# Optimization experiments

Hardware: AMD Instinct MI355X
Metric: run time of the kernel (lower is better)

## Reference

```python
import jax, jax.numpy as jnp
import numpy as np

TOP_K = 2  # matches init k


def setup_inputs() -> dict:
    key = jax.random.key(0)
    ks = jax.random.split(key, 5)
    B, S, D, E, H = 2, 2048, 1024, 8, 4096
    scale = 0.02
    return {
        "x": jax.random.normal(ks[0], (B, S, D), dtype=jnp.float32),
        "wg": jax.random.normal(ks[1], (D, E), dtype=jnp.float32) * scale,
        "w1": jax.random.normal(ks[2], (E, D, H), dtype=jnp.float32) * scale,
        "w3": jax.random.normal(ks[3], (E, D, H), dtype=jnp.float32) * scale,
        "w2": jax.random.normal(ks[4], (E, H, D), dtype=jnp.float32) * scale,
    }


def reference(x, wg, w1, w3, w2):
    # x: [B, S, D]; wg: [D, E]; w1/w3: [E, D, H]; w2: [E, H, D]
    B, S, D = x.shape
    E = wg.shape[1]
    T = B * S
    xt = x.reshape(T, D)

    # Top-k gating: softmax over expert logits, keep top-k, renormalize.
    logits = xt @ wg                                    # [T, E]
    probs = jax.nn.softmax(logits, axis=-1)             # [T, E]
    topv, topi = jax.lax.top_k(probs, TOP_K)            # [T, k]
    topv = topv / topv.sum(axis=-1, keepdims=True)
    # Dense combine weights [T, E] (zero for non-selected experts).
    comb = jnp.zeros((T, E), dtype=x.dtype).at[jnp.arange(T)[:, None], topi].set(topv)

    # Per-expert SwiGLU MLP with weighted combine (loop over small fixed E).
    out = jnp.zeros_like(xt)
    for e in range(E):
        h = jax.nn.silu(xt @ w1[e]) * (xt @ w3[e])      # [T, H]
        out = out + comb[:, e:e + 1] * (h @ w2[e])       # [T, D]
    return out.reshape(B, S, D)
```

## Files before the change

kernel.cpp:

```cpp
#include <hip/hip_runtime.h>
#include <cstdint>
#include <cstddef>

#define T_TOK 4096
#define DIM   1024
#define NEXP  8
#define HDIM  4096
#define NSLOT (2 * T_TOK)

#define BM 128
#define BN 128
#define BK 32

typedef __attribute__((ext_vector_type(8))) short s16x8;
typedef __attribute__((ext_vector_type(4))) float f32x4;

__device__ __forceinline__ unsigned short f2bf(float f) {
    union { float f; unsigned u; } v; v.f = f;
    unsigned u = v.u;
    unsigned r = (u + 0x7FFFu + ((u >> 16) & 1u)) >> 16;
    return (unsigned short)r;
}

__device__ __forceinline__ int lds_off(int row, int kchunk) {
    return row * 32 + ((kchunk ^ ((row >> 1) & 3)) << 3);
}

__device__ __forceinline__ void gload16(const void* g, void* l) {
    __builtin_amdgcn_global_load_lds(
        (const __attribute__((address_space(1))) unsigned int*)g,
        (__attribute__((address_space(3))) unsigned int*)l, 16, 0, 0);
}

__global__ __launch_bounds__(256) void gate_kernel(
    const float* __restrict__ x, const float* __restrict__ wg,
    int* __restrict__ tok_e, float* __restrict__ tok_w, int* __restrict__ counts)
{
    int t = blockIdx.x * 4 + (threadIdx.x >> 6);
    int lane = threadIdx.x & 63;
    float acc[NEXP];
#pragma unroll
    for (int e = 0; e < NEXP; ++e) acc[e] = 0.f;
    const float* xrow = x + (size_t)t * DIM;
    for (int d = lane; d < DIM; d += 64) {
        float xv = xrow[d];
        const float4* wr = (const float4*)(wg + (size_t)d * NEXP);
        float4 w0 = wr[0], w1v = wr[1];
        acc[0] += xv * w0.x;  acc[1] += xv * w0.y;
        acc[2] += xv * w0.z;  acc[3] += xv * w0.w;
        acc[4] += xv * w1v.x; acc[5] += xv * w1v.y;
        acc[6] += xv * w1v.z; acc[7] += xv * w1v.w;
    }
#pragma unroll
    for (int e = 0; e < NEXP; ++e)
#pragma unroll
        for (int off = 32; off > 0; off >>= 1)
            acc[e] += __shfl_xor(acc[e], off);
    if (lane == 0) {
        int i0 = 0;
#pragma unroll
        for (int e = 1; e < NEXP; ++e) if (acc[e] > acc[i0]) i0 = e;
        int i1 = (i0 == 0) ? 1 : 0;
#pragma unroll
        for (int e = 0; e < NEXP; ++e) if (e != i0 && acc[e] > acc[i1]) i1 = e;
        float w0 = 1.f / (1.f + __expf(acc[i1] - acc[i0]));
        tok_e[2 * t] = i0;  tok_e[2 * t + 1] = i1;
        tok_w[2 * t] = w0;  tok_w[2 * t + 1] = 1.f - w0;
        atomicAdd(&counts[i0], 1);
        atomicAdd(&counts[i1], 1);
    }
}

__global__ void scan_kernel(const int* __restrict__ counts,
                            int* __restrict__ offsets, int* __restrict__ cursor)
{
    if (threadIdx.x == 0) {
        int s = 0;
        for (int e = 0; e < NEXP; ++e) { offsets[e] = s; s += counts[e]; cursor[e] = 0; }
        offsets[NEXP] = s;
    }
}

__global__ __launch_bounds__(256) void assign_kernel(
    const int* __restrict__ tok_e,
    const int* __restrict__ offsets, int* __restrict__ cursor,
    int* __restrict__ rows_tok, int* __restrict__ slot_of)
{
    int t = blockIdx.x * 256 + threadIdx.x;
    if (t >= T_TOK) return;
#pragma unroll
    for (int j = 0; j < 2; ++j) {
        int e = tok_e[2 * t + j];
        int pos = offsets[e] + atomicAdd(&cursor[e], 1);
        rows_tok[pos] = t;
        slot_of[2 * t + j] = pos;
    }
}

__global__ __launch_bounds__(256) void xconv_kernel(
    const float* __restrict__ x, const int* __restrict__ rows_tok,
    unsigned short* __restrict__ xg)
{
    int slot = blockIdx.x;
    int tok = rows_tok[slot];
    int d = threadIdx.x * 4;
    float4 v = *(const float4*)(x + (size_t)tok * DIM + d);
    ushort4 o;
    o.x = f2bf(v.x); o.y = f2bf(v.y); o.z = f2bf(v.z); o.w = f2bf(v.w);
    *(ushort4*)(xg + (size_t)slot * DIM + d) = o;
}

__global__ __launch_bounds__(256) void tconv_kernel(
    const float* __restrict__ src, unsigned short* __restrict__ dst, int R, int C)
{
    __shared__ unsigned int t_lds[64 * 33];
    int e = blockIdx.z;
    int c0 = blockIdx.x * 64, r0 = blockIdx.y * 64;
    int t = threadIdx.x;
    int lane = t & 63, w = t >> 6;
    const float* s = src + (size_t)e * R * C + (size_t)(r0 + w * 16) * C + c0 + lane;
#pragma unroll
    for (int j = 0; j < 8; ++j) {
        float v0 = s[(size_t)(2 * j) * C];
        float v1 = s[(size_t)(2 * j + 1) * C];
        unsigned int pk = (unsigned int)f2bf(v0) | ((unsigned int)f2bf(v1) << 16);
        t_lds[lane * 33 + (w * 8 + j)] = pk;
    }
    __syncthreads();
    unsigned short* dbase = dst + (size_t)e * C * R;
#pragma unroll
    for (int rep = 0; rep < 2; ++rep) {
        int idx = rep * 256 + t;
        int c = idx >> 3, chunk = idx & 7;
        uint4 o;
        o.x = t_lds[c * 33 + chunk * 4 + 0];
        o.y = t_lds[c * 33 + chunk * 4 + 1];
        o.z = t_lds[c * 33 + chunk * 4 + 2];
        o.w = t_lds[c * 33 + chunk * 4 + 3];
        *(uint4*)(dbase + (size_t)(c0 + c) * R + r0 + chunk * 8) = o;
    }
}

__global__ __launch_bounds__(512, 4) void gemm1_kernel(
    const unsigned short* __restrict__ xg,
    const unsigned short* __restrict__ w1t, const unsigned short* __restrict__ w3t,
    const int* __restrict__ offsets, unsigned short* __restrict__ h)
{
    int e = blockIdx.z;
    int offs = offsets[e];
    int cnt  = offsets[e + 1] - offs;
    int m0 = blockIdx.y * BM;
    if (m0 >= cnt) return;
    int n0 = blockIdx.x * BN;

    __shared__ unsigned short As[2][BM * BK];
    __shared__ unsigned short B1s[2][BN * BK];
    __shared__ unsigned short B3s[2][BN * BK];

    int tid = threadIdx.x;
    int lane = tid & 63;
    int wid = tid >> 6;
    int wr = wid >> 2, wc = wid & 3;
    int lr = lane & 15, lg = lane >> 4;

    int srow = tid >> 2;
    int g = (tid & 3) ^ ((srow >> 1) & 3);
    int arow = offs + min(m0 + srow, cnt - 1);
    const unsigned short* asrc  = xg  + (size_t)arow * DIM + g * 8;
    const unsigned short* b1src = w1t + ((size_t)e * HDIM + n0 + srow) * DIM + g * 8;
    const unsigned short* b3src = w3t + ((size_t)e * HDIM + n0 + srow) * DIM + g * 8;
    int ldsbase = wid * 512;

    f32x4 acc1[4][2] = {};
    f32x4 acc3[4][2] = {};

    auto stage = [&](int buf, int k0) {
        gload16(asrc + k0,  &As[buf][ldsbase]);
        gload16(b1src + k0, &B1s[buf][ldsbase]);
        gload16(b3src + k0, &B3s[buf][ldsbase]);
    };

    auto compute = [&](int buf) {
        s16x8 a[4];
#pragma unroll
        for (int m = 0; m < 4; ++m)
            a[m] = *(const s16x8*)&As[buf][lds_off(wr * 64 + m * 16 + lr, lg)];
#pragma unroll
        for (int n = 0; n < 2; ++n) {
            int rowb = wc * 32 + n * 16 + lr;
            s16x8 b1f = *(const s16x8*)&B1s[buf][lds_off(rowb, lg)];
            s16x8 b3f = *(const s16x8*)&B3s[buf][lds_off(rowb, lg)];
#pragma unroll
            for (int m = 0; m < 4; ++m)
                acc1[m][n] = __builtin_amdgcn_mfma_f32_16x16x32_bf16(a[m], b1f, acc1[m][n], 0, 0, 0);
#pragma unroll
            for (int m = 0; m < 4; ++m)
                acc3[m][n] = __builtin_amdgcn_mfma_f32_16x16x32_bf16(a[m], b3f, acc3[m][n], 0, 0, 0);
        }
    };

    stage(0, 0);
    __syncthreads();
    int buf = 0;
    for (int kt = 1; kt < DIM / BK; ++kt) {
        stage(buf ^ 1, kt * BK);
        compute(buf);
        __syncthreads();
        buf ^= 1;
    }
    compute(buf);

#pragma unroll
    for (int m = 0; m < 4; ++m)
#pragma unroll
        for (int n = 0; n < 2; ++n)
#pragma unroll
            for (int r = 0; r < 4; ++r) {
                int row_local = wr * 64 + m * 16 + lg * 4 + r;
                if (m0 + row_local < cnt) {
                    int col_local = wc * 32 + n * 16 + lr;
                    float g1 = acc1[m][n][r];
                    float hv = (g1 / (1.f + __expf(-g1))) * acc3[m][n][r];
                    h[(size_t)(offs + m0 + row_local) * HDIM + n0 + col_local] = f2bf(hv);
                }
            }
}

__global__ __launch_bounds__(512, 4) void gemm2_kernel(
    const unsigned short* __restrict__ h, const unsigned short* __restrict__ w2t,
    const int* __restrict__ offsets, float* __restrict__ outg)
{
    int e = blockIdx.z;
    int offs = offsets[e];
    int cnt  = offsets[e + 1] - offs;
    int m0 = blockIdx.y * BM;
    if (m0 >= cnt) return;
    int n0 = blockIdx.x * BN;

    __shared__ unsigned short As[2][BM * BK];
    __shared__ unsigned short Bs[2][BN * BK];

    int tid = threadIdx.x;
    int lane = tid & 63;
    int wid = tid >> 6;
    int wr = wid >> 2, wc = wid & 3;
    int lr = lane & 15, lg = lane >> 4;

    int srow = tid >> 2;
    int g = (tid & 3) ^ ((srow >> 1) & 3);
    int arow = offs + min(m0 + srow, cnt - 1);
    const unsigned short* asrc = h   + (size_t)arow * HDIM + g * 8;
    const unsigned short* bsrc = w2t + ((size_t)e * DIM + n0 + srow) * HDIM + g * 8;
    int ldsbase = wid * 512;

    f32x4 acc[4][2] = {};

    auto stage = [&](int buf, int k0) {
        gload16(asrc + k0, &As[buf][ldsbase]);
        gload16(bsrc + k0, &Bs[buf][ldsbase]);
    };

    auto compute = [&](int buf) {
        s16x8 a[4];
#pragma unroll
        for (int m = 0; m < 4; ++m)
            a[m] = *(const s16x8*)&As[buf][lds_off(wr * 64 + m * 16 + lr, lg)];
#pragma unroll
        for (int n = 0; n < 2; ++n) {
            s16x8 bf = *(const s16x8*)&Bs[buf][lds_off(wc * 32 + n * 16 + lr, lg)];
#pragma unroll
            for (int m = 0; m < 4; ++m)
                acc[m][n] = __builtin_amdgcn_mfma_f32_16x16x32_bf16(a[m], bf, acc[m][n], 0, 0, 0);
        }
    };

    stage(0, 0);
    __syncthreads();
    int buf = 0;
    for (int kt = 1; kt < HDIM / BK; ++kt) {
        stage(buf ^ 1, kt * BK);
        compute(buf);
        __syncthreads();
        buf ^= 1;
    }
    compute(buf);

#pragma unroll
    for (int m = 0; m < 4; ++m)
#pragma unroll
        for (int n = 0; n < 2; ++n)
#pragma unroll
            for (int r = 0; r < 4; ++r) {
                int row_local = wr * 64 + m * 16 + lg * 4 + r;
                if (m0 + row_local < cnt) {
                    int col_local = wc * 32 + n * 16 + lr;
                    outg[(size_t)(offs + m0 + row_local) * DIM + n0 + col_local] = acc[m][n][r];
                }
            }
}

__global__ __launch_bounds__(256) void combine_kernel(
    const float* __restrict__ outg, const int* __restrict__ slot_of,
    const float* __restrict__ tok_w, float* __restrict__ out)
{
    int t = blockIdx.x;
    int s0 = slot_of[2 * t], s1 = slot_of[2 * t + 1];
    float g0 = tok_w[2 * t], g1 = tok_w[2 * t + 1];
    int d = threadIdx.x * 4;
    float4 a = *(const float4*)(outg + (size_t)s0 * DIM + d);
    float4 b = *(const float4*)(outg + (size_t)s1 * DIM + d);
    float4 o;
    o.x = g0 * a.x + g1 * b.x;
    o.y = g0 * a.y + g1 * b.y;
    o.z = g0 * a.z + g1 * b.z;
    o.w = g0 * a.w + g1 * b.w;
    *(float4*)(out + (size_t)t * DIM + d) = o;
}

extern "C" void kernel_launch(void* const* d_in, const int* in_sizes, int n_in,
                              void* d_out, int out_size, void* d_ws, size_t ws_size,
                              hipStream_t stream)
{
    const float* x  = (const float*)d_in[0];
    const float* wg = (const float*)d_in[1];
    const float* w1 = (const float*)d_in[2];
    const float* w3 = (const float*)d_in[3];
    const float* w2 = (const float*)d_in[4];
    float* out = (float*)d_out;

    char* ws = (char*)d_ws;
    size_t off = 0;
    auto alloc = [&](size_t bytes) -> void* {
        void* p = ws + off;
        off = (off + bytes + 255) & ~(size_t)255;
        return p;
    };
    int*   rows_tok = (int*)alloc((size_t)NSLOT * 4);
    int*   slot_of  = (int*)alloc((size_t)NSLOT * 4);
    int*   tok_e    = (int*)alloc((size_t)NSLOT * 4);
    float* tok_w    = (float*)alloc((size_t)NSLOT * 4);
    int*   counts   = (int*)alloc(NEXP * 4);
    int*   offsets  = (int*)alloc((NEXP + 1) * 4);
    int*   cursor   = (int*)alloc(NEXP * 4);
    unsigned short* xg   = (unsigned short*)alloc((size_t)NSLOT * DIM * 2);
    unsigned short* w1t  = (unsigned short*)alloc((size_t)NEXP * HDIM * DIM * 2);
    unsigned short* w3t  = (unsigned short*)alloc((size_t)NEXP * HDIM * DIM * 2);
    unsigned short* hbuf = (unsigned short*)alloc((size_t)NSLOT * HDIM * 2);
    unsigned short* w2t  = w1t;
    float*          outg = (float*)w3t;

    hipMemsetAsync(counts, 0, NEXP * 4, stream);

    gate_kernel<<<T_TOK / 4, 256, 0, stream>>>(x, wg, tok_e, tok_w, counts);
    scan_kernel<<<1, 64, 0, stream>>>(counts, offsets, cursor);
    assign_kernel<<<T_TOK / 256, 256, 0, stream>>>(tok_e, offsets, cursor,
                                                   rows_tok, slot_of);
    xconv_kernel<<<NSLOT, 256, 0, stream>>>(x, rows_tok, xg);

    tconv_kernel<<<dim3(HDIM / 64, DIM / 64, NEXP), 256, 0, stream>>>(w1, w1t, DIM, HDIM);
    tconv_kernel<<<dim3(HDIM / 64, DIM / 64, NEXP), 256, 0, stream>>>(w3, w3t, DIM, HDIM);

    gemm1_kernel<<<dim3(HDIM / BN, T_TOK / BM, NEXP), 512, 0, stream>>>(
        xg, w1t, w3t, offsets, hbuf);

    tconv_kernel<<<dim3(DIM / 64, HDIM / 64, NEXP), 256, 0, stream>>>(w2, w2t, HDIM, DIM);

    gemm2_kernel<<<dim3(DIM / BN, T_TOK / BM, NEXP), 512, 0, stream>>>(
        hbuf, w2t, offsets, outg);

    combine_kernel<<<T_TOK, 256, 0, stream>>>(outg, slot_of, tok_w, out);
}
```

Baseline: 576.6 us.

## Fuse bf16 x conversion into gating, gather rows in GEMM1, scatter-add combine in GEMM2

```diff
diff --git a/kernel.cpp b/kernel.cpp
--- a/kernel.cpp
+++ b/kernel.cpp
@@ -9,7 +9,8 @@
 #define NSLOT (2 * T_TOK)
 
 #define BM 128
-#define BN 128
+#define BN1 128
+#define BN2 256
 #define BK 32
 
 typedef __attribute__((ext_vector_type(8))) short s16x8;
@@ -34,7 +35,8 @@
 
 __global__ __launch_bounds__(256) void gate_kernel(
     const float* __restrict__ x, const float* __restrict__ wg,
-    int* __restrict__ tok_e, float* __restrict__ tok_w, int* __restrict__ counts)
+    int* __restrict__ tok_e, float* __restrict__ tok_w, int* __restrict__ counts,
+    unsigned short* __restrict__ xg)
 {
     int t = blockIdx.x * 4 + (threadIdx.x >> 6);
     int lane = threadIdx.x & 63;
@@ -42,8 +44,10 @@
 #pragma unroll
     for (int e = 0; e < NEXP; ++e) acc[e] = 0.f;
     const float* xrow = x + (size_t)t * DIM;
+    unsigned short* xgrow = xg + (size_t)t * DIM;
     for (int d = lane; d < DIM; d += 64) {
         float xv = xrow[d];
+        xgrow[d] = f2bf(xv);
         const float4* wr = (const float4*)(wg + (size_t)d * NEXP);
         float4 w0 = wr[0], w1v = wr[1];
         acc[0] += xv * w0.x;  acc[1] += xv * w0.y;
@@ -82,9 +86,9 @@
 }
 
 __global__ __launch_bounds__(256) void assign_kernel(
-    const int* __restrict__ tok_e,
+    const int* __restrict__ tok_e, const float* __restrict__ tok_w,
     const int* __restrict__ offsets, int* __restrict__ cursor,
-    int* __restrict__ rows_tok, int* __restrict__ slot_of)
+    int* __restrict__ rows_tok, float* __restrict__ rows_gate)
 {
     int t = blockIdx.x * 256 + threadIdx.x;
     if (t >= T_TOK) return;
@@ -93,30 +97,16 @@
         int e = tok_e[2 * t + j];
         int pos = offsets[e] + atomicAdd(&cursor[e], 1);
         rows_tok[pos] = t;
-        slot_of[2 * t + j] = pos;
-    }
-}
-
-__global__ __launch_bounds__(256) void xconv_kernel(
-    const float* __restrict__ x, const int* __restrict__ rows_tok,
-    unsigned short* __restrict__ xg)
-{
-    int slot = blockIdx.x;
-    int tok = rows_tok[slot];
-    int d = threadIdx.x * 4;
-    float4 v = *(const float4*)(x + (size_t)tok * DIM + d);
-    ushort4 o;
-    o.x = f2bf(v.x); o.y = f2bf(v.y); o.z = f2bf(v.z); o.w = f2bf(v.w);
-    *(ushort4*)(xg + (size_t)slot * DIM + d) = o;
-}
-
-__global__ __launch_bounds__(256) void tconv_kernel(
-    const float* __restrict__ src, unsigned short* __restrict__ dst, int R, int C)
+        rows_gate[pos] = tok_w[2 * t + j];
+    }
+}
+
+__device__ __forceinline__ void tconv_body(
+    const float* __restrict__ src, unsigned short* __restrict__ dst,
+    int R, int C, int e, int bx, int by, int t)
 {
     __shared__ unsigned int t_lds[64 * 33];
-    int e = blockIdx.z;
-    int c0 = blockIdx.x * 64, r0 = blockIdx.y * 64;
-    int t = threadIdx.x;
+    int c0 = bx * 64, r0 = by * 64;
     int lane = t & 63, w = t >> 6;
     const float* s = src + (size_t)e * R * C + (size_t)(r0 + w * 16) * C + c0 + lane;
 #pragma unroll
@@ -141,23 +131,45 @@
     }
 }
 
+__global__ __launch_bounds__(256) void tconv13_kernel(
+    const float* __restrict__ w1, const float* __restrict__ w3,
+    unsigned short* __restrict__ w1t, unsigned short* __restrict__ w3t)
+{
+    int z = blockIdx.z;
+    if (z < NEXP)
+        tconv_body(w1, w1t, DIM, HDIM, z, blockIdx.x, blockIdx.y, threadIdx.x);
+    else
+        tconv_body(w3, w3t, DIM, HDIM, z - NEXP, blockIdx.x, blockIdx.y, threadIdx.x);
+}
+
+__global__ __launch_bounds__(256) void tconv_kernel(
+    const float* __restrict__ src, unsigned short* __restrict__ dst, int R, int C)
+{
+    tconv_body(src, dst, R, C, blockIdx.z, blockIdx.x, blockIdx.y, threadIdx.x);
+}
+
 __global__ __launch_bounds__(512, 4) void gemm1_kernel(
     const unsigned short* __restrict__ xg,
     const unsigned short* __restrict__ w1t, const unsigned short* __restrict__ w3t,
-    const int* __restrict__ offsets, unsigned short* __restrict__ h)
+    const int* __restrict__ rows_tok, const int* __restrict__ offsets,
+    unsigned short* __restrict__ h)
 {
     int e = blockIdx.z;
     int offs = offsets[e];
     int cnt  = offsets[e + 1] - offs;
     int m0 = blockIdx.y * BM;
     if (m0 >= cnt) return;
-    int n0 = blockIdx.x * BN;
+    int n0 = blockIdx.x * BN1;
 
     __shared__ unsigned short As[2][BM * BK];
-    __shared__ unsigned short B1s[2][BN * BK];
-    __shared__ unsigned short B3s[2][BN * BK];
+    __shared__ unsigned short B1s[2][BN1 * BK];
+    __shared__ unsigned short B3s[2][BN1 * BK];
+    __shared__ int toks[BM];
 
     int tid = threadIdx.x;
+    if (tid < BM) toks[tid] = rows_tok[offs + min(m0 + tid, cnt - 1)];
+    __syncthreads();
+
     int lane = tid & 63;
     int wid = tid >> 6;
     int wr = wid >> 2, wc = wid & 3;
@@ -165,8 +177,7 @@
 
     int srow = tid >> 2;
     int g = (tid & 3) ^ ((srow >> 1) & 3);
-    int arow = offs + min(m0 + srow, cnt - 1);
-    const unsigned short* asrc  = xg  + (size_t)arow * DIM + g * 8;
+    const unsigned short* asrc  = xg  + (size_t)toks[srow] * DIM + g * 8;
     const unsigned short* b1src = w1t + ((size_t)e * HDIM + n0 + srow) * DIM + g * 8;
     const unsigned short* b3src = w3t + ((size_t)e * HDIM + n0 + srow) * DIM + g * 8;
     int ldsbase = wid * 512;
@@ -228,19 +239,28 @@
 
 __global__ __launch_bounds__(512, 4) void gemm2_kernel(
     const unsigned short* __restrict__ h, const unsigned short* __restrict__ w2t,
-    const int* __restrict__ offsets, float* __restrict__ outg)
+    const int* __restrict__ rows_tok, const float* __restrict__ rows_gate,
+    const int* __restrict__ offsets, float* __restrict__ out)
 {
     int e = blockIdx.z;
     int offs = offsets[e];
     int cnt  = offsets[e + 1] - offs;
     int m0 = blockIdx.y * BM;
     if (m0 >= cnt) return;
-    int n0 = blockIdx.x * BN;
+    int n0 = blockIdx.x * BN2;
 
     __shared__ unsigned short As[2][BM * BK];
-    __shared__ unsigned short Bs[2][BN * BK];
+    __shared__ unsigned short Bs[2][BN2 * BK];
+    __shared__ int   toks[BM];
+    __shared__ float gts[BM];
 
     int tid = threadIdx.x;
+    if (tid < BM) {
+        int p = offs + min(m0 + tid, cnt - 1);
+        toks[tid] = rows_tok[p];
+        gts[tid]  = rows_gate[p];
+    }
+
     int lane = tid & 63;
     int wid = tid >> 6;
     int wr = wid >> 2, wc = wid & 3;
@@ -249,15 +269,17 @@
     int srow = tid >> 2;
     int g = (tid & 3) ^ ((srow >> 1) & 3);
     int arow = offs + min(m0 + srow, cnt - 1);
-    const unsigned short* asrc = h   + (size_t)arow * HDIM + g * 8;
-    const unsigned short* bsrc = w2t + ((size_t)e * DIM + n0 + srow) * HDIM + g * 8;
-    int ldsbase = wid * 512;
-
-    f32x4 acc[4][2] = {};
+    const unsigned short* asrc = h + (size_t)arow * HDIM + g * 8;
+    const unsigned short* bsrc0 = w2t + ((size_t)e * DIM + n0 + srow) * HDIM + g * 8;
+    const unsigned short* bsrc1 = w2t + ((size_t)e * DIM + n0 + 128 + srow) * HDIM + g * 8;
+    int ldsA = wid * 512;
+
+    f32x4 acc[4][4] = {};
 
     auto stage = [&](int buf, int k0) {
-        gload16(asrc + k0, &As[buf][ldsbase]);
-        gload16(bsrc + k0, &Bs[buf][ldsbase]);
+        gload16(asrc + k0,  &As[buf][ldsA]);
+        gload16(bsrc0 + k0, &Bs[buf][ldsA]);
+        gload16(bsrc1 + k0, &Bs[buf][4096 + ldsA]);
     };
 
     auto compute = [&](int buf) {
@@ -266,14 +288,15 @@
         for (int m = 0; m < 4; ++m)
             a[m] = *(const s16x8*)&As[buf][lds_off(wr * 64 + m * 16 + lr, lg)];
 #pragma unroll
-        for (int n = 0; n < 2; ++n) {
-            s16x8 bf = *(const s16x8*)&Bs[buf][lds_off(wc * 32 + n * 16 + lr, lg)];
+        for (int n = 0; n < 4; ++n) {
+            s16x8 bf = *(const s16x8*)&Bs[buf][lds_off(wc * 64 + n * 16 + lr, lg)];
 #pragma unroll
             for (int m = 0; m < 4; ++m)
                 acc[m][n] = __builtin_amdgcn_mfma_f32_16x16x32_bf16(a[m], bf, acc[m][n], 0, 0, 0);
         }
     };
 
+    __syncthreads();
     stage(0, 0);
     __syncthreads();
     int buf = 0;
@@ -288,33 +311,16 @@
 #pragma unroll
     for (int m = 0; m < 4; ++m)
 #pragma unroll
-        for (int n = 0; n < 2; ++n)
+        for (int n = 0; n < 4; ++n)
 #pragma unroll
             for (int r = 0; r < 4; ++r) {
                 int row_local = wr * 64 + m * 16 + lg * 4 + r;
                 if (m0 + row_local < cnt) {
-                    int col_local = wc * 32 + n * 16 + lr;
-                    outg[(size_t)(offs + m0 + row_local) * DIM + n0 + col_local] = acc[m][n][r];
+                    int col = n0 + wc * 64 + n * 16 + lr;
+                    float v = acc[m][n][r] * gts[row_local];
+                    atomicAdd(&out[(size_t)toks[row_local] * DIM + col], v);
                 }
             }
-}
-
-__global__ __launch_bounds__(256) void combine_kernel(
-    const float* __restrict__ outg, const int* __restrict__ slot_of,
-    const float* __restrict__ tok_w, float* __restrict__ out)
-{
-    int t = blockIdx.x;
-    int s0 = slot_of[2 * t], s1 = slot_of[2 * t + 1];
-    float g0 = tok_w[2 * t], g1 = tok_w[2 * t + 1];
-    int d = threadIdx.x * 4;
-    float4 a = *(const float4*)(outg + (size_t)s0 * DIM + d);
-    float4 b = *(const float4*)(outg + (size_t)s1 * DIM + d);
-    float4 o;
-    o.x = g0 * a.x + g1 * b.x;
-    o.y = g0 * a.y + g1 * b.y;
-    o.z = g0 * a.z + g1 * b.z;
-    o.w = g0 * a.w + g1 * b.w;
-    *(float4*)(out + (size_t)t * DIM + d) = o;
 }
 
 extern "C" void kernel_launch(void* const* d_in, const int* in_sizes, int n_in,
@@ -335,38 +341,35 @@
         off = (off + bytes + 255) & ~(size_t)255;
         return p;
     };
-    int*   rows_tok = (int*)alloc((size_t)NSLOT * 4);
-    int*   slot_of  = (int*)alloc((size_t)NSLOT * 4);
-    int*   tok_e    = (int*)alloc((size_t)NSLOT * 4);
-    float* tok_w    = (float*)alloc((size_t)NSLOT * 4);
-    int*   counts   = (int*)alloc(NEXP * 4);
-    int*   offsets  = (int*)alloc((NEXP + 1) * 4);
-    int*   cursor   = (int*)alloc(NEXP * 4);
-    unsigned short* xg   = (unsigned short*)alloc((size_t)NSLOT * DIM * 2);
+    int*   rows_tok  = (int*)alloc((size_t)NSLOT * 4);
+    float* rows_gate = (float*)alloc((size_t)NSLOT * 4);
+    int*   tok_e     = (int*)alloc((size_t)NSLOT * 4);
+    float* tok_w     = (float*)alloc((size_t)NSLOT * 4);
+    int*   counts    = (int*)alloc(NEXP * 4);
+    int*   offsets   = (int*)alloc((NEXP + 1) * 4);
+    int*   cursor    = (int*)alloc(NEXP * 4);
+    unsigned short* xg   = (unsigned short*)alloc((size_t)T_TOK * DIM * 2);
     unsigned short* w1t  = (unsigned short*)alloc((size_t)NEXP * HDIM * DIM * 2);
     unsigned short* w3t  = (unsigned short*)alloc((size_t)NEXP * HDIM * DIM * 2);
     unsigned short* hbuf = (unsigned short*)alloc((size_t)NSLOT * HDIM * 2);
     unsigned short* w2t  = w1t;
-    float*          outg = (float*)w3t;
 
     hipMemsetAsync(counts, 0, NEXP * 4, stream);
-
-    gate_kernel<<<T_TOK / 4, 256, 0, stream>>>(x, wg, tok_e, tok_w, counts);
+    hipMemsetAsync(out, 0, (size_t)out_size * sizeof(float), stream);
+
+    gate_kernel<<<T_TOK / 4, 256, 0, stream>>>(x, wg, tok_e, tok_w, counts, xg);
     scan_kernel<<<1, 64, 0, stream>>>(counts, offsets, cursor);
-    assign_kernel<<<T_TOK / 256, 256, 0, stream>>>(tok_e, offsets, cursor,
-                                                   rows_tok, slot_of);
-    xconv_kernel<<<NSLOT, 256, 0, stream>>>(x, rows_tok, xg);
-
-    tconv_kernel<<<dim3(HDIM / 64, DIM / 64, NEXP), 256, 0, stream>>>(w1, w1t, DIM, HDIM);
-    tconv_kernel<<<dim3(HDIM / 64, DIM / 64, NEXP), 256, 0, stream>>>(w3, w3t, DIM, HDIM);
-
-    gemm1_kernel<<<dim3(HDIM / BN, T_TOK / BM, NEXP), 512, 0, stream>>>(
-        xg, w1t, w3t, offsets, hbuf);
+    assign_kernel<<<T_TOK / 256, 256, 0, stream>>>(tok_e, tok_w, offsets, cursor,
+                                                   rows_tok, rows_gate);
+
+    tconv13_kernel<<<dim3(HDIM / 64, DIM / 64, 2 * NEXP), 256, 0, stream>>>(
+        w1, w3, w1t, w3t);
+
+    gemm1_kernel<<<dim3(HDIM / BN1, T_TOK / BM, NEXP), 512, 0, stream>>>(
+        xg, w1t, w3t, rows_tok, offsets, hbuf);
 
     tconv_kernel<<<dim3(DIM / 64, HDIM / 64, NEXP), 256, 0, stream>>>(w2, w2t, HDIM, DIM);
 
-    gemm2_kernel<<<dim3(DIM / BN, T_TOK / BM, NEXP), 512, 0, stream>>>(
-        hbuf, w2t, offsets, outg);
-
-    combine_kernel<<<T_TOK, 256, 0, stream>>>(outg, slot_of, tok_w, out);
-}
+    gemm2_kernel<<<dim3(DIM / BN2, T_TOK / BM, NEXP), 512, 0, stream>>>(
+        hbuf, w2t, rows_tok, rows_gate, offsets, out);
+}
```

Result: no change. 580.8 us (+0.7%).
